# Optimization experiments

Measured on AMD Instinct MI355X. Metric: run time of the kernel, lower is better.

## Reference

```python
import jax, jax.numpy as jnp
import numpy as np

B = 1024        # graphs per batch
NPG = 64        # nodes per graph (uniform)
DEG = 16        # avg degree
NE_PG = 256     # candidate non-edges per graph
N = B * NPG
E = N * DEG
NE = B * NE_PG
EMB, HID, NCAT, NET, NOUT = 64, 128, 100, 4, 101  # NOUT = num_external + 1


def setup_inputs() -> dict:
    key = jax.random.key(0)
    ks = jax.random.split(key, 32)
    rn = lambda k, shape: jax.random.normal(k, shape, jnp.float32) * 0.05
    # graph structure: edges and non-edges stay within each graph's node block
    x = jax.random.randint(ks[0], (N,), 0, NCAT)
    offs = jnp.repeat(jnp.arange(B) * NPG, NPG * DEG)
    src = jax.random.randint(ks[1], (E,), 0, NPG) + offs
    dst = jax.random.randint(ks[2], (E,), 0, NPG) + offs
    edge_index = jnp.stack([src, dst])
    edge_attr = jax.random.randint(ks[3], (E,), 0, NET)
    offs_ne = jnp.repeat(jnp.arange(B) * NPG, NE_PG)
    non_edges = jax.random.randint(ks[4], (NE, 2), 0, NPG) + offs_ne[:, None]
    batch = jnp.repeat(jnp.arange(B), NPG)
    return dict(
        node_tab=rn(ks[5], (NCAT, EMB)), edge_tab=rn(ks[6], (NET, EMB)),
        c1_w=rn(ks[7], (EMB, HID)), c1_we=rn(ks[8], (EMB, HID)),
        c1_as=rn(ks[9], (HID,)), c1_ad=rn(ks[10], (HID,)), c1_ae=rn(ks[11], (HID,)), c1_b=rn(ks[12], (HID,)),
        c2_w=rn(ks[13], (HID, HID)), c2_we=rn(ks[14], (EMB, HID)),
        c2_as=rn(ks[15], (HID,)), c2_ad=rn(ks[16], (HID,)), c2_ae=rn(ks[17], (HID,)), c2_b=rn(ks[18], (HID,)),
        s_w1=rn(ks[19], (HID, HID)), s_b1=rn(ks[20], (HID,)), s_w2=rn(ks[21], (HID, 1)), s_b2=rn(ks[22], (1,)),
        n_w1=rn(ks[23], (HID, HID)), n_b1=rn(ks[24], (HID,)), n_w2=rn(ks[25], (HID, NOUT)), n_b2=rn(ks[26], (NOUT,)),
        e_w1=rn(ks[27], (HID, HID)), e_b1=rn(ks[28], (HID,)), e_w2=rn(ks[29], (HID, 1)), e_b2=rn(ks[30], (1,)),
        x=x, edge_index=edge_index, edge_attr=edge_attr, non_edges=non_edges, batch=batch,
    )


def _gat(h_in, src, dst, e, W, We, a_s, a_d, a_e, b):
    """PyG GATConv, heads=1: gather -> leakyrelu logits -> segment softmax over dst -> scatter sum."""
    n = h_in.shape[0]
    h = h_in @ W                  # [N, C]
    he = e @ We                   # [E, C]
    logit = (h @ a_s)[src] + (h @ a_d)[dst] + he @ a_e   # [E]
    logit = jnp.where(logit > 0, logit, 0.2 * logit)      # leaky_relu(0.2)
    m = jax.ops.segment_max(logit, dst, num_segments=n)
    ex = jnp.exp(logit - m[dst])
    den = jax.ops.segment_sum(ex, dst, num_segments=n)
    alpha = ex / (den[dst] + 1e-16)
    return jax.ops.segment_sum(h[src] * alpha[:, None], dst, num_segments=n) + b


def _mlp(z, w1, b1, w2, b2):
    return jax.nn.relu(z @ w1 + b1) @ w2 + b2


def reference(node_tab, edge_tab,
              c1_w, c1_we, c1_as, c1_ad, c1_ae, c1_b,
              c2_w, c2_we, c2_as, c2_ad, c2_ae, c2_b,
              s_w1, s_b1, s_w2, s_b2,
              n_w1, n_b1, n_w2, n_b2,
              e_w1, e_b1, e_w2, e_b2,
              x, edge_index, edge_attr, non_edges, batch):
    src, dst = edge_index[0], edge_index[1]
    e = edge_tab[edge_attr]                      # [E, EMB]
    h = node_tab[x]                              # [N, EMB]
    h = jax.nn.relu(_gat(h, src, dst, e, c1_w, c1_we, c1_as, c1_ad, c1_ae, c1_b))
    h = _gat(h, src, dst, e, c2_w, c2_we, c2_as, c2_ad, c2_ae, c2_b)   # [N, HID]
    g = jax.ops.segment_sum(h, batch, num_segments=B)                   # [B, HID]
    stop = _mlp(g, s_w1, s_b1, s_w2, s_b2)                              # [B, 1]
    addnode = _mlp(h, n_w1, n_b1, n_w2, n_b2)                           # [N, NOUT]
    pair = h[non_edges[:, 0]] + h[non_edges[:, 1]]                      # [NE, HID]
    addedge = _mlp(pair, e_w1, e_b1, e_w2, e_b2)                        # [NE, 1]
    # uniform per-graph sizes -> the torch split/pad is a static reshape+concat
    return jnp.concatenate(
        [stop, addnode.reshape(B, NPG * NOUT), addedge.reshape(B, NE_PG)], axis=1)
```

## Files before the change

### kernel.cpp

```cpp
#include <hip/hip_runtime.h>
#include <hip/hip_bf16.h>


#define NPG 64
#define EPG 1024
#define NEPG 256
#define B_GR 1024
#define E_TOT 1048576
#define EMB 64
#define HID 128
#define NOUT 101
#define OUT_PG 6721

typedef __attribute__((ext_vector_type(8))) short bf16x8;
typedef __attribute__((ext_vector_type(4))) float f32x4;
typedef unsigned short ushort_t;

__device__ ushort_t g_nt1[100*HID];
__device__ ushort_t g_c2w[HID*HID];
__device__ ushort_t g_nw1[HID*HID];
__device__ ushort_t g_ew1[HID*HID];
__device__ ushort_t g_nw2[HID*112];
__device__ float    g_sw1t[HID*HID];
__device__ float    g_hs1[128], g_hd1[128];
__device__ float    g_he1[4], g_he2[4];

__device__ __forceinline__ ushort_t f2bf(float f) {
  unsigned u = __float_as_uint(f);
  return (ushort_t)((u + 0x7fffu + ((u >> 16) & 1u)) >> 16);
}
__device__ __forceinline__ float bf2f(ushort_t h) {
  return __uint_as_float(((unsigned)h) << 16);
}
__device__ __forceinline__ unsigned pk2(float a, float b) {
  __hip_bfloat162 h = __float22bfloat162_rn(make_float2(a, b));
  unsigned r; __builtin_memcpy(&r, &h, 4); return r;
}
__device__ __forceinline__ bf16x8 pk8(float4 v0, float4 v1) {
  union { bf16x8 v; unsigned u[4]; } o;
  o.u[0] = pk2(v0.x, v0.y); o.u[1] = pk2(v0.z, v0.w);
  o.u[2] = pk2(v1.x, v1.y); o.u[3] = pk2(v1.z, v1.w);
  return o.v;
}

__global__ void prep_kernel(
    const float* __restrict__ node_tab, const float* __restrict__ edge_tab,
    const float* __restrict__ c1_w,  const float* __restrict__ c1_we,
    const float* __restrict__ c1_as, const float* __restrict__ c1_ad,
    const float* __restrict__ c1_ae,
    const float* __restrict__ c2_w,  const float* __restrict__ c2_we,
    const float* __restrict__ c2_ae,
    const float* __restrict__ s_w1,  const float* __restrict__ n_w1,
    const float* __restrict__ n_w2,  const float* __restrict__ e_w1)
{
  const int b = blockIdx.x, tid = threadIdx.x;
  if (b == 0) {
    __shared__ float v1[EMB], v2[EMB];
    if (tid < EMB) {
      float a = 0.f, d = 0.f;
      for (int j = 0; j < HID; ++j) {
        a = fmaf(c1_we[tid*HID + j], c1_ae[j], a);
        d = fmaf(c2_we[tid*HID + j], c2_ae[j], d);
      }
      v1[tid] = a; v2[tid] = d;
    }
    __syncthreads();
    if (tid < 4) {
      float a = 0.f, d = 0.f;
      for (int k = 0; k < EMB; ++k) {
        const float ev = edge_tab[tid*EMB + k];
        a = fmaf(ev, v1[k], a); d = fmaf(ev, v2[k], d);
      }
      g_he1[tid] = a; g_he2[tid] = d;
    }
    return;
  }
  if (b <= 50) {
    const int idx = (b - 1) * 256 + tid;
    const int i = idx >> 7, j = idx & (HID - 1);
    float s = 0.f;
    #pragma unroll 8
    for (int k = 0; k < EMB; ++k) s = fmaf(node_tab[i*EMB + k], c1_w[k*HID + j], s);
    g_nt1[idx] = f2bf(s);
    return;
  }
  if (b == 51) {
    __shared__ float vs[EMB], vd[EMB];
    if (tid < EMB) {
      float a = 0.f, d = 0.f;
      for (int j = 0; j < HID; ++j) {
        const float w = c1_w[tid*HID + j];
        a = fmaf(w, c1_as[j], a); d = fmaf(w, c1_ad[j], d);
      }
      vs[tid] = a; vd[tid] = d;
    }
    __syncthreads();
    if (tid < 128) {
      float a = 0.f, d = 0.f;
      if (tid < 100) {
        for (int k = 0; k < EMB; ++k) {
          const float xv = node_tab[tid*EMB + k];
          a = fmaf(xv, vs[k], a); d = fmaf(xv, vd[k], d);
        }
      }
      g_hs1[tid] = a; g_hd1[tid] = d;
    }
    return;
  }
  if (b <= 75) {
    const int grp = (b - 52) >> 3;
    const int chunk = (b - 52) & 7;
    const float* W = (grp == 0) ? c2_w : (grp == 1) ? n_w1 : e_w1;
    ushort_t* G = (grp == 0) ? g_c2w : (grp == 1) ? g_nw1 : g_ew1;
    const int base = chunk * 2048 + tid;
    #pragma unroll
    for (int it = 0; it < 8; ++it) {
      const int idx = base + it*256;
      const int j = idx & 7, l = (idx >> 3) & 63, r2 = idx >> 9;
      const int ks = r2 & 3, ct = r2 >> 2;
      const int row = ks*32 + (l >> 4)*8 + j;
      const int col = ct*16 + (l & 15);
      G[idx] = f2bf(W[row*HID + col]);
    }
    return;
  }
  if (b <= 82) {
    const int base = (b - 76) * 2048 + tid;
    #pragma unroll
    for (int it = 0; it < 8; ++it) {
      const int idx = base + it*256;
      const int j = idx & 7, l = (idx >> 3) & 63, r2 = idx >> 9;
      const int ks = r2 & 3, ct = r2 >> 2;
      const int row = ks*32 + (l >> 4)*8 + j;
      const int col = ct*16 + (l & 15);
      g_nw2[idx] = (col < NOUT) ? f2bf(n_w2[row*NOUT + col]) : (ushort_t)0;
    }
    return;
  }
  {
    const int base = (b - 83) * 2048 + tid;
    #pragma unroll
    for (int it = 0; it < 8; ++it) {
      const int idx = base + it*256;
      g_sw1t[idx] = s_w1[(idx & 127)*HID + (idx >> 7)];
    }
  }
}

#define S_HC   0
#define S_R    18432
#define S_PART 35840
#define S_NS   36864
#define S_ND   37120
#define S_GP   37376
#define S_EBW  37888
#define S_HCC  38912
#define S_XS   38944
#define S_TOT  39200

__global__ __launch_bounds__(256, 4) void graph_kernel(
    const float* __restrict__ c1_b,
    const float* __restrict__ c2_as, const float* __restrict__ c2_ad,
    const float* __restrict__ c2_b,
    const float* __restrict__ s_b1,  const float* __restrict__ s_w2,
    const float* __restrict__ s_b2,
    const float* __restrict__ n_b1,  const float* __restrict__ n_b2,
    const float* __restrict__ e_b1,  const float* __restrict__ e_w2,
    const float* __restrict__ e_b2,
    const int* __restrict__ x,  const int* __restrict__ ei,
    const int* __restrict__ ea, const int* __restrict__ nedg,
    float* __restrict__ out)
{
  const int tid = threadIdx.x;
  const int gid = blockIdx.x;
  const int nb = gid * NPG;
  const int lane = tid & 63;
  const int wv = tid >> 6;
  const int qd = lane >> 4;
  const int cl = lane & 15;
  const int rb = wv * 16;

  __shared__ __align__(16) char smem[S_TOT];
  ushort_t* Hc   = (ushort_t*)(smem + S_HC);
  float*    Pf   = (float*)   (smem + S_R);
  ushort_t* Hr   = (ushort_t*)(smem + S_R);
  float*    part = (float*)   (smem + S_PART);
  float*    ns   = (float*)   (smem + S_NS);
  float*    nd   = (float*)   (smem + S_ND);
  float*    gp   = (float*)   (smem + S_GP);
  float*    ebw  = (float*)   (smem + S_EBW);
  float*    hc   = (float*)   (smem + S_HCC);
  int*      xs   = (int*)     (smem + S_XS);
  ushort_t* a1b  = Hc;

  unsigned er[4];
  #pragma unroll
  for (int i = 0; i < 4; ++i) {
    const int k = tid + 256*i;
    const int s = ei[gid*EPG + k] - nb;
    const int d = ei[E_TOT + gid*EPG + k] - nb;
    const int t = ea[gid*EPG + k];
    er[i] = (unsigned)(s | (d << 6) | (t << 12));
  }
  const int2 prr = *(const int2*)(nedg + 2*(gid*NEPG + tid));
  if (tid < NPG) {
    const int cat = x[nb + tid];
    xs[tid] = cat;
    ns[tid] = g_hs1[cat];
    nd[tid] = g_hd1[cat];
  }
  {
    float4* pz = (float4*)Pf;
    #pragma unroll
    for (int j = 0; j < 4; ++j) pz[tid + j*256] = make_float4(0.f,0.f,0.f,0.f);
  }
  if (tid < 128) gp[tid] = 0.f;
  ebw[tid] = (tid < 128) ? e_b1[tid] : e_w2[tid - 128];
  if (tid < 8) hc[tid] = (tid < 4) ? g_he1[tid] : g_he2[tid-4];
  __syncthreads();

  {
    const int gn = tid >> 2;
    const int f0 = (tid & 3) * 32;
    const ushort_t* srcp = g_nt1 + xs[gn]*HID + f0;
    const bf16x8 t0 = ((const bf16x8*)srcp)[0];
    const bf16x8 t1 = ((const bf16x8*)srcp)[1];
    const bf16x8 t2 = ((const bf16x8*)srcp)[2];
    const bf16x8 t3 = ((const bf16x8*)srcp)[3];
    #pragma unroll
    for (int i = 0; i < 4; ++i) {
      const unsigned tp = er[i];
      const int s = tp & 63, d = (tp >> 6) & 63, t = tp >> 12;
      float l = ns[s] + nd[d] + hc[t];
      l = (l > 0.f) ? l : 0.2f * l;
      atomicAdd(&Pf[d*64 + s], __expf(l));
    }
    #pragma unroll
    for (int q = 0; q < 8; ++q) {
      Hc[(f0 +      q)*72 + gn] = (ushort_t)t0[q];
      Hc[(f0 +  8 + q)*72 + gn] = (ushort_t)t1[q];
      Hc[(f0 + 16 + q)*72 + gn] = (ushort_t)t2[q];
      Hc[(f0 + 24 + q)*72 + gn] = (ushort_t)t3[q];
    }
  }
  __syncthreads();

  bf16x8 pa0, pa1;
  float inv4[4];
  {
    const float* pr = Pf + (rb + cl)*64;
    const float4 v0 = *(const float4*)(pr + qd*8);
    const float4 v1 = *(const float4*)(pr + qd*8 + 4);
    const float4 v2 = *(const float4*)(pr + 32 + qd*8);
    const float4 v3 = *(const float4*)(pr + 36 + qd*8);
    pa0 = pk8(v0, v1); pa1 = pk8(v2, v3);
    float den = v0.x+v0.y+v0.z+v0.w + v1.x+v1.y+v1.z+v1.w
              + v2.x+v2.y+v2.z+v2.w + v3.x+v3.y+v3.z+v3.w;
    den += __shfl_xor(den, 16, 64);
    den += __shfl_xor(den, 32, 64);
    #pragma unroll
    for (int r = 0; r < 4; ++r)
      inv4[r] = 1.f / (__shfl(den, qd*4 + r, 64) + 1e-16f);
  }
  __syncthreads();

  {
    #pragma unroll
    for (int ct = 0; ct < 8; ++ct) {
      f32x4 acc = {0.f, 0.f, 0.f, 0.f};
      const bf16x8 b0 = *(const bf16x8*)(Hc + (ct*16+cl)*72 + qd*8);
      const bf16x8 b1 = *(const bf16x8*)(Hc + (ct*16+cl)*72 + 32 + qd*8);
      acc = __builtin_amdgcn_mfma_f32_16x16x32_bf16(pa0, b0, acc, 0, 0, 0);
      acc = __builtin_amdgcn_mfma_f32_16x16x32_bf16(pa1, b1, acc, 0, 0, 0);
      const int n = ct*16 + cl;
      const float bias = c1_b[n];
      #pragma unroll
      for (int r = 0; r < 4; ++r)
        Hr[(rb + qd*4 + r)*136 + n] = f2bf(fmaxf(fmaf(acc[r], inv4[r], bias), 0.f));
    }
  }
  bf16x8 h1f[4];
  #pragma unroll
  for (int ks = 0; ks < 4; ++ks)
    h1f[ks] = *(const bf16x8*)(Hr + (rb+cl)*136 + ks*32 + qd*8);
  __syncthreads();

  {
    float4* pz = (float4*)Pf;
    #pragma unroll
    for (int j = 0; j < 4; ++j) pz[tid + j*256] = make_float4(0.f,0.f,0.f,0.f);
    float pns[4] = {0.f,0.f,0.f,0.f}, pnd[4] = {0.f,0.f,0.f,0.f};
    #pragma unroll
    for (int ct = 0; ct < 8; ++ct) {
      f32x4 acc = {0.f, 0.f, 0.f, 0.f};
      #pragma unroll
      for (int ks = 0; ks < 4; ++ks) {
        const bf16x8 b = *(const bf16x8*)(g_c2w + ((ct*4+ks)*64 + lane)*8);
        acc = __builtin_amdgcn_mfma_f32_16x16x32_bf16(h1f[ks], b, acc, 0, 0, 0);
      }
      const int n = ct*16 + cl;
      const float asv = c2_as[n], adv = c2_ad[n];
      #pragma unroll
      for (int r = 0; r < 4; ++r) {
        const float v = acc[r];
        Hc[n*72 + (rb + qd*4 + r)] = f2bf(v);
        pns[r] = fmaf(v, asv, pns[r]);
        pnd[r] = fmaf(v, adv, pnd[r]);
      }
    }
    #pragma unroll
    for (int r = 0; r < 4; ++r) {
      #pragma unroll
      for (int off = 1; off < 16; off <<= 1) {
        pns[r] += __shfl_xor(pns[r], off, 64);
        pnd[r] += __shfl_xor(pnd[r], off, 64);
      }
    }
    if (cl == 0) {
      #pragma unroll
      for (int r = 0; r < 4; ++r) { ns[rb+qd*4+r] = pns[r]; nd[rb+qd*4+r] = pnd[r]; }
    }
  }
  __syncthreads();

  #pragma unroll
  for (int i = 0; i < 4; ++i) {
    const unsigned tp = er[i];
    const int s = tp & 63, d = (tp >> 6) & 63, t = tp >> 12;
    float l = ns[s] + nd[d] + hc[4 + t];
    l = (l > 0.f) ? l : 0.2f * l;
    atomicAdd(&Pf[d*64 + s], __expf(l));
  }
  __syncthreads();

  {
    const float* pr = Pf + (rb + cl)*64;
    const float4 v0 = *(const float4*)(pr + qd*8);
    const float4 v1 = *(const float4*)(pr + qd*8 + 4);
    const float4 v2 = *(const float4*)(pr + 32 + qd*8);
    const float4 v3 = *(const float4*)(pr + 36 + qd*8);
    pa0 = pk8(v0, v1); pa1 = pk8(v2, v3);
    float den = v0.x+v0.y+v0.z+v0.w + v1.x+v1.y+v1.z+v1.w
              + v2.x+v2.y+v2.z+v2.w + v3.x+v3.y+v3.z+v3.w;
    den += __shfl_xor(den, 16, 64);
    den += __shfl_xor(den, 32, 64);
    #pragma unroll
    for (int r = 0; r < 4; ++r)
      inv4[r] = 1.f / (__shfl(den, qd*4 + r, 64) + 1e-16f);
  }
  __syncthreads();

  {
    #pragma unroll
    for (int ct = 0; ct < 8; ++ct) {
      f32x4 acc = {0.f, 0.f, 0.f, 0.f};
      const bf16x8 b0 = *(const bf16x8*)(Hc + (ct*16+cl)*72 + qd*8);
      const bf16x8 b1 = *(const bf16x8*)(Hc + (ct*16+cl)*72 + 32 + qd*8);
      acc = __builtin_amdgcn_mfma_f32_16x16x32_bf16(pa0, b0, acc, 0, 0, 0);
      acc = __builtin_amdgcn_mfma_f32_16x16x32_bf16(pa1, b1, acc, 0, 0, 0);
      const int n = ct*16 + cl;
      const float bias = c2_b[n];
      float colsum = 0.f;
      #pragma unroll
      for (int r = 0; r < 4; ++r) {
        const float v = fmaf(acc[r], inv4[r], bias);
        Hr[(rb + qd*4 + r)*136 + n] = f2bf(v);
        colsum += v;
      }
      colsum += __shfl_xor(colsum, 16, 64);
      colsum += __shfl_xor(colsum, 32, 64);
      if (qd == 0) atomicAdd(&gp[n], colsum);
    }
  }
  __syncthreads();

  {
    const int j = tid & 127, half = tid >> 7;
    const float* wr = g_sw1t + j*HID + half*64;
    const float* gr = gp + half*64;
    float p = 0.f;
    #pragma unroll
    for (int q = 0; q < 16; ++q) {
      const float4 w = ((const float4*)wr)[q];
      const float4 g = ((const float4*)gr)[q];
      p = fmaf(w.x, g.x, p); p = fmaf(w.y, g.y, p);
      p = fmaf(w.z, g.z, p); p = fmaf(w.w, g.w, p);
    }
    part[tid] = p;
  }
  __syncthreads();

  if (tid < 64) {
    const float z0 = fmaxf(part[tid] + part[tid+128] + s_b1[tid], 0.f);
    const float z1 = fmaxf(part[tid+64] + part[tid+192] + s_b1[tid+64], 0.f);
    float p = fmaf(z0, s_w2[tid], z1 * s_w2[tid+64]);
    #pragma unroll
    for (int off = 32; off > 0; off >>= 1) p += __shfl_down(p, off, 64);
    if (tid == 0) out[(size_t)gid*OUT_PG] = p + s_b2[0];
  }

  bf16x8 h2f[4];
  #pragma unroll
  for (int ks = 0; ks < 4; ++ks)
    h2f[ks] = *(const bf16x8*)(Hr + (rb+cl)*136 + ks*32 + qd*8);

  {
    #pragma unroll
    for (int ct = 0; ct < 8; ++ct) {
      f32x4 an = {0.f, 0.f, 0.f, 0.f};
      f32x4 ae2 = {0.f, 0.f, 0.f, 0.f};
      #pragma unroll
      for (int ks = 0; ks < 4; ++ks) {
        const bf16x8 bn = *(const bf16x8*)(g_nw1 + ((ct*4+ks)*64 + lane)*8);
        const bf16x8 be = *(const bf16x8*)(g_ew1 + ((ct*4+ks)*64 + lane)*8);
        an  = __builtin_amdgcn_mfma_f32_16x16x32_bf16(h2f[ks], bn, an, 0, 0, 0);
        ae2 = __builtin_amdgcn_mfma_f32_16x16x32_bf16(h2f[ks], be, ae2, 0, 0, 0);
      }
      const int n = ct*16 + cl;
      const float bias = n_b1[n];
      #pragma unroll
      for (int r = 0; r < 4; ++r) {
        a1b[(rb + qd*4 + r)*136 + n] = f2bf(fmaxf(an[r] + bias, 0.f));
        Hr[(rb + qd*4 + r)*136 + n] = f2bf(ae2[r]);
      }
    }
  }
  {
    bf16x8 af[4];
    #pragma unroll
    for (int ks = 0; ks < 4; ++ks)
      af[ks] = *(const bf16x8*)(a1b + (rb+cl)*136 + ks*32 + qd*8);
    float* ob = out + (size_t)gid*OUT_PG + 1;
    #pragma unroll
    for (int ct = 0; ct < 7; ++ct) {
      f32x4 acc = {0.f, 0.f, 0.f, 0.f};
      #pragma unroll
      for (int ks = 0; ks < 4; ++ks) {
        const bf16x8 b = *(const bf16x8*)(g_nw2 + ((ct*4+ks)*64 + lane)*8);
        acc = __builtin_amdgcn_mfma_f32_16x16x32_bf16(af[ks], b, acc, 0, 0, 0);
      }
      const int o = ct*16 + cl;
      if (o < NOUT) {
        const float b2 = n_b2[o];
        #pragma unroll
        for (int r = 0; r < 4; ++r)
          ob[(size_t)(rb + qd*4 + r)*NOUT + o] = acc[r] + b2;
      }
    }
  }
  __syncthreads();

  {
    const ushort_t* ui = Hr + (prr.x - nb)*136;
    const ushort_t* uj = Hr + (prr.y - nb)*136;
    float ssum = 0.f;
    #pragma unroll
    for (int q8 = 0; q8 < 16; ++q8) {
      const bf16x8 va = *(const bf16x8*)(ui + q8*8);
      const bf16x8 vb = *(const bf16x8*)(uj + q8*8);
      #pragma unroll
      for (int j = 0; j < 8; ++j) {
        const int c = q8*8 + j;
        float v = bf2f((ushort_t)va[j]) + bf2f((ushort_t)vb[j]) + ebw[c];
        v = fmaxf(v, 0.f);
        ssum = fmaf(v, ebw[128 + c], ssum);
      }
    }
    out[(size_t)gid*OUT_PG + 1 + NPG*NOUT + tid] = ssum + e_b2[0];
  }
}

extern "C" void kernel_launch(void* const* d_in, const int* in_sizes, int n_in,
                              void* d_out, int out_size, void* d_ws, size_t ws_size,
                              hipStream_t stream) {
  const float* node_tab = (const float*)d_in[0];
  const float* edge_tab = (const float*)d_in[1];
  const float* c1_w  = (const float*)d_in[2];
  const float* c1_we = (const float*)d_in[3];
  const float* c1_as = (const float*)d_in[4];
  const float* c1_ad = (const float*)d_in[5];
  const float* c1_ae = (const float*)d_in[6];
  const float* c1_b  = (const float*)d_in[7];
  const float* c2_w  = (const float*)d_in[8];
  const float* c2_we = (const float*)d_in[9];
  const float* c2_as = (const float*)d_in[10];
  const float* c2_ad = (const float*)d_in[11];
  const float* c2_ae = (const float*)d_in[12];
  const float* c2_b  = (const float*)d_in[13];
  const float* s_w1  = (const float*)d_in[14];
  const float* s_b1  = (const float*)d_in[15];
  const float* s_w2  = (const float*)d_in[16];
  const float* s_b2  = (const float*)d_in[17];
  const float* n_w1  = (const float*)d_in[18];
  const float* n_b1  = (const float*)d_in[19];
  const float* n_w2  = (const float*)d_in[20];
  const float* n_b2  = (const float*)d_in[21];
  const float* e_w1  = (const float*)d_in[22];
  const float* e_b1  = (const float*)d_in[23];
  const float* e_w2  = (const float*)d_in[24];
  const float* e_b2  = (const float*)d_in[25];
  const int* x    = (const int*)d_in[26];
  const int* ei   = (const int*)d_in[27];
  const int* ea   = (const int*)d_in[28];
  const int* nedg = (const int*)d_in[29];
  float* out = (float*)d_out;

  prep_kernel<<<dim3(91), dim3(256), 0, stream>>>(
      node_tab, edge_tab, c1_w, c1_we, c1_as, c1_ad, c1_ae,
      c2_w, c2_we, c2_ae, s_w1, n_w1, n_w2, e_w1);

  graph_kernel<<<dim3(B_GR), dim3(256), 0, stream>>>(
      c1_b, c2_as, c2_ad, c2_b, s_b1, s_w2, s_b2,
      n_b1, n_b2, e_b1, e_w2, e_b2, x, ei, ea, nedg, out);
}
```

Before: 185.5 us.

## Double block to 512 threads splitting column tiles across wave pairs, swizzle score matrix

Doubles the per-graph thread block from 256 to 512 threads. Each pair of wave groups now handles half the output column tiles in every MFMA stage, and the per-edge, non-edge and stop-MLP work is split over twice as many threads, with partial sums combined through atomics, shuffles or extra reductions. It also XOR-swizzles the attention score matrix layout in shared memory to cut bank conflicts on the atomic adds and row reads. The aim is more parallelism per graph to hide latency, at the cost of extra barriers, some shared-memory atomics, and launch bounds asking for 8 blocks per CU, which tightens register limits.

```diff
diff --git a/kernel.cpp b/kernel.cpp
--- a/kernel.cpp
+++ b/kernel.cpp
@@ -41,6 +41,9 @@
   o.u[0] = pk2(v0.x, v0.y); o.u[1] = pk2(v0.z, v0.w);
   o.u[2] = pk2(v1.x, v1.y); o.u[3] = pk2(v1.z, v1.w);
   return o.v;
+}
+__device__ __forceinline__ int pf_idx(int d, int s) {
+  return d*64 + ((((s >> 2) ^ d) & 15) << 2) + (s & 3);
 }
 
 __global__ void prep_kernel(
@@ -150,15 +153,15 @@
 #define S_HC   0
 #define S_R    18432
 #define S_PART 35840
-#define S_NS   36864
-#define S_ND   37120
-#define S_GP   37376
-#define S_EBW  37888
-#define S_HCC  38912
-#define S_XS   38944
-#define S_TOT  39200
-
-__global__ __launch_bounds__(256, 4) void graph_kernel(
+#define S_NS   37888
+#define S_ND   38144
+#define S_GP   38400
+#define S_EBW  38912
+#define S_HCC  39936
+#define S_XS   39968
+#define S_TOT  40224
+
+__global__ __launch_bounds__(512, 8) void graph_kernel(
     const float* __restrict__ c1_b,
     const float* __restrict__ c2_as, const float* __restrict__ c2_ad,
     const float* __restrict__ c2_b,
@@ -176,9 +179,11 @@
   const int nb = gid * NPG;
   const int lane = tid & 63;
   const int wv = tid >> 6;
+  const int wr = wv & 3;
+  const int ch = wv >> 2;
   const int qd = lane >> 4;
   const int cl = lane & 15;
-  const int rb = wv * 16;
+  const int rb = wr * 16;
 
   __shared__ __align__(16) char smem[S_TOT];
   ushort_t* Hc   = (ushort_t*)(smem + S_HC);
@@ -193,16 +198,16 @@
   int*      xs   = (int*)     (smem + S_XS);
   ushort_t* a1b  = Hc;
 
-  unsigned er[4];
+  unsigned er[2];
   #pragma unroll
-  for (int i = 0; i < 4; ++i) {
-    const int k = tid + 256*i;
+  for (int i = 0; i < 2; ++i) {
+    const int k = tid + 512*i;
     const int s = ei[gid*EPG + k] - nb;
     const int d = ei[E_TOT + gid*EPG + k] - nb;
     const int t = ea[gid*EPG + k];
     er[i] = (unsigned)(s | (d << 6) | (t << 12));
   }
-  const int2 prr = *(const int2*)(nedg + 2*(gid*NEPG + tid));
+  const int2 prr = *(const int2*)(nedg + 2*(gid*NEPG + (tid >> 1)));
   if (tid < NPG) {
     const int cat = x[nb + tid];
     xs[tid] = cat;
@@ -211,36 +216,31 @@
   }
   {
     float4* pz = (float4*)Pf;
-    #pragma unroll
-    for (int j = 0; j < 4; ++j) pz[tid + j*256] = make_float4(0.f,0.f,0.f,0.f);
+    pz[tid]       = make_float4(0.f,0.f,0.f,0.f);
+    pz[tid + 512] = make_float4(0.f,0.f,0.f,0.f);
   }
   if (tid < 128) gp[tid] = 0.f;
-  ebw[tid] = (tid < 128) ? e_b1[tid] : e_w2[tid - 128];
+  if (tid < 256) ebw[tid] = (tid < 128) ? e_b1[tid] : e_w2[tid - 128];
   if (tid < 8) hc[tid] = (tid < 4) ? g_he1[tid] : g_he2[tid-4];
   __syncthreads();
 
   {
-    const int gn = tid >> 2;
-    const int f0 = (tid & 3) * 32;
-    const ushort_t* srcp = g_nt1 + xs[gn]*HID + f0;
+    const int f0 = wv * 16;
+    const ushort_t* srcp = g_nt1 + xs[lane]*HID + f0;
     const bf16x8 t0 = ((const bf16x8*)srcp)[0];
     const bf16x8 t1 = ((const bf16x8*)srcp)[1];
-    const bf16x8 t2 = ((const bf16x8*)srcp)[2];
-    const bf16x8 t3 = ((const bf16x8*)srcp)[3];
-    #pragma unroll
-    for (int i = 0; i < 4; ++i) {
+    #pragma unroll
+    for (int i = 0; i < 2; ++i) {
       const unsigned tp = er[i];
       const int s = tp & 63, d = (tp >> 6) & 63, t = tp >> 12;
       float l = ns[s] + nd[d] + hc[t];
       l = (l > 0.f) ? l : 0.2f * l;
-      atomicAdd(&Pf[d*64 + s], __expf(l));
+      atomicAdd(&Pf[pf_idx(d, s)], __expf(l));
     }
     #pragma unroll
     for (int q = 0; q < 8; ++q) {
-      Hc[(f0 +      q)*72 + gn] = (ushort_t)t0[q];
-      Hc[(f0 +  8 + q)*72 + gn] = (ushort_t)t1[q];
-      Hc[(f0 + 16 + q)*72 + gn] = (ushort_t)t2[q];
-      Hc[(f0 + 24 + q)*72 + gn] = (ushort_t)t3[q];
+      Hc[(f0 +     q)*72 + lane] = (ushort_t)t0[q];
+      Hc[(f0 + 8 + q)*72 + lane] = (ushort_t)t1[q];
     }
   }
   __syncthreads();
@@ -249,10 +249,10 @@
   float inv4[4];
   {
     const float* pr = Pf + (rb + cl)*64;
-    const float4 v0 = *(const float4*)(pr + qd*8);
-    const float4 v1 = *(const float4*)(pr + qd*8 + 4);
-    const float4 v2 = *(const float4*)(pr + 32 + qd*8);
-    const float4 v3 = *(const float4*)(pr + 36 + qd*8);
+    const float4 v0 = *(const float4*)(pr + (((2*qd    ) ^ cl) << 2));
+    const float4 v1 = *(const float4*)(pr + (((2*qd + 1) ^ cl) << 2));
+    const float4 v2 = *(const float4*)(pr + (((2*qd + 8) ^ cl) << 2));
+    const float4 v3 = *(const float4*)(pr + (((2*qd + 9) ^ cl) << 2));
     pa0 = pk8(v0, v1); pa1 = pk8(v2, v3);
     float den = v0.x+v0.y+v0.z+v0.w + v1.x+v1.y+v1.z+v1.w
               + v2.x+v2.y+v2.z+v2.w + v3.x+v3.y+v3.z+v3.w;
@@ -262,11 +262,13 @@
     for (int r = 0; r < 4; ++r)
       inv4[r] = 1.f / (__shfl(den, qd*4 + r, 64) + 1e-16f);
   }
-  __syncthreads();
-
-  {
-    #pragma unroll
-    for (int ct = 0; ct < 8; ++ct) {
+  if (tid < NPG) { ns[tid] = 0.f; nd[tid] = 0.f; }
+  __syncthreads();
+
+  {
+    #pragma unroll
+    for (int i = 0; i < 4; ++i) {
+      const int ct = ch*4 + i;
       f32x4 acc = {0.f, 0.f, 0.f, 0.f};
       const bf16x8 b0 = *(const bf16x8*)(Hc + (ct*16+cl)*72 + qd*8);
       const bf16x8 b1 = *(const bf16x8*)(Hc + (ct*16+cl)*72 + 32 + qd*8);
@@ -279,6 +281,7 @@
         Hr[(rb + qd*4 + r)*136 + n] = f2bf(fmaxf(fmaf(acc[r], inv4[r], bias), 0.f));
     }
   }
+  __syncthreads();
   bf16x8 h1f[4];
   #pragma unroll
   for (int ks = 0; ks < 4; ++ks)
@@ -287,11 +290,12 @@
 
   {
     float4* pz = (float4*)Pf;
-    #pragma unroll
-    for (int j = 0; j < 4; ++j) pz[tid + j*256] = make_float4(0.f,0.f,0.f,0.f);
+    pz[tid]       = make_float4(0.f,0.f,0.f,0.f);
+    pz[tid + 512] = make_float4(0.f,0.f,0.f,0.f);
     float pns[4] = {0.f,0.f,0.f,0.f}, pnd[4] = {0.f,0.f,0.f,0.f};
     #pragma unroll
-    for (int ct = 0; ct < 8; ++ct) {
+    for (int i = 0; i < 4; ++i) {
+      const int ct = ch*4 + i;
       f32x4 acc = {0.f, 0.f, 0.f, 0.f};
       #pragma unroll
       for (int ks = 0; ks < 4; ++ks) {
@@ -318,27 +322,30 @@
     }
     if (cl == 0) {
       #pragma unroll
-      for (int r = 0; r < 4; ++r) { ns[rb+qd*4+r] = pns[r]; nd[rb+qd*4+r] = pnd[r]; }
+      for (int r = 0; r < 4; ++r) {
+        atomicAdd(&ns[rb + qd*4 + r], pns[r]);
+        atomicAdd(&nd[rb + qd*4 + r], pnd[r]);
+      }
     }
   }
   __syncthreads();
 
   #pragma unroll
-  for (int i = 0; i < 4; ++i) {
+  for (int i = 0; i < 2; ++i) {
     const unsigned tp = er[i];
     const int s = tp & 63, d = (tp >> 6) & 63, t = tp >> 12;
     float l = ns[s] + nd[d] + hc[4 + t];
     l = (l > 0.f) ? l : 0.2f * l;
-    atomicAdd(&Pf[d*64 + s], __expf(l));
+    atomicAdd(&Pf[pf_idx(d, s)], __expf(l));
   }
   __syncthreads();
 
   {
     const float* pr = Pf + (rb + cl)*64;
-    const float4 v0 = *(const float4*)(pr + qd*8);
-    const float4 v1 = *(const float4*)(pr + qd*8 + 4);
-    const float4 v2 = *(const float4*)(pr + 32 + qd*8);
-    const float4 v3 = *(const float4*)(pr + 36 + qd*8);
+    const float4 v0 = *(const float4*)(pr + (((2*qd    ) ^ cl) << 2));
+    const float4 v1 = *(const float4*)(pr + (((2*qd + 1) ^ cl) << 2));
+    const float4 v2 = *(const float4*)(pr + (((2*qd + 8) ^ cl) << 2));
+    const float4 v3 = *(const float4*)(pr + (((2*qd + 9) ^ cl) << 2));
     pa0 = pk8(v0, v1); pa1 = pk8(v2, v3);
     float den = v0.x+v0.y+v0.z+v0.w + v1.x+v1.y+v1.z+v1.w
               + v2.x+v2.y+v2.z+v2.w + v3.x+v3.y+v3.z+v3.w;
@@ -352,7 +359,8 @@
 
   {
     #pragma unroll
-    for (int ct = 0; ct < 8; ++ct) {
+    for (int i = 0; i < 4; ++i) {
+      const int ct = ch*4 + i;
       f32x4 acc = {0.f, 0.f, 0.f, 0.f};
       const bf16x8 b0 = *(const bf16x8*)(Hc + (ct*16+cl)*72 + qd*8);
       const bf16x8 b1 = *(const bf16x8*)(Hc + (ct*16+cl)*72 + 32 + qd*8);
@@ -375,39 +383,41 @@
   __syncthreads();
 
   {
-    const int j = tid & 127, half = tid >> 7;
-    const float* wr = g_sw1t + j*HID + half*64;
-    const float* gr = gp + half*64;
+    const int j = tid & 127, c = tid >> 7;
+    const float* wrp = g_sw1t + j*HID + c*32;
+    const float* grp = gp + c*32;
     float p = 0.f;
     #pragma unroll
-    for (int q = 0; q < 16; ++q) {
-      const float4 w = ((const float4*)wr)[q];
-      const float4 g = ((const float4*)gr)[q];
+    for (int q = 0; q < 8; ++q) {
+      const float4 w = ((const float4*)wrp)[q];
+      const float4 g = ((const float4*)grp)[q];
       p = fmaf(w.x, g.x, p); p = fmaf(w.y, g.y, p);
       p = fmaf(w.z, g.z, p); p = fmaf(w.w, g.w, p);
     }
     part[tid] = p;
   }
-  __syncthreads();
-
-  if (tid < 64) {
-    const float z0 = fmaxf(part[tid] + part[tid+128] + s_b1[tid], 0.f);
-    const float z1 = fmaxf(part[tid+64] + part[tid+192] + s_b1[tid+64], 0.f);
-    float p = fmaf(z0, s_w2[tid], z1 * s_w2[tid+64]);
-    #pragma unroll
-    for (int off = 32; off > 0; off >>= 1) p += __shfl_down(p, off, 64);
-    if (tid == 0) out[(size_t)gid*OUT_PG] = p + s_b2[0];
-  }
-
   bf16x8 h2f[4];
   #pragma unroll
   for (int ks = 0; ks < 4; ++ks)
     h2f[ks] = *(const bf16x8*)(Hr + (rb+cl)*136 + ks*32 + qd*8);
-
-  {
-    #pragma unroll
-    for (int ct = 0; ct < 8; ++ct) {
-      f32x4 an = {0.f, 0.f, 0.f, 0.f};
+  __syncthreads();
+
+  if (tid < 64) {
+    const float d0 = part[tid]    + part[tid+128] + part[tid+256] + part[tid+384];
+    const float d1 = part[tid+64] + part[tid+192] + part[tid+320] + part[tid+448];
+    const float z0 = fmaxf(d0 + s_b1[tid], 0.f);
+    const float z1 = fmaxf(d1 + s_b1[tid+64], 0.f);
+    float p = fmaf(z0, s_w2[tid], z1 * s_w2[tid+64]);
+    #pragma unroll
+    for (int off = 32; off > 0; off >>= 1) p += __shfl_down(p, off, 64);
+    if (tid == 0) out[(size_t)gid*OUT_PG] = p + s_b2[0];
+  }
+
+  {
+    #pragma unroll
+    for (int i = 0; i < 4; ++i) {
+      const int ct = ch*4 + i;
+      f32x4 an  = {0.f, 0.f, 0.f, 0.f};
       f32x4 ae2 = {0.f, 0.f, 0.f, 0.f};
       #pragma unroll
       for (int ks = 0; ks < 4; ++ks) {
@@ -425,6 +435,8 @@
       }
     }
   }
+  __syncthreads();
+
   {
     bf16x8 af[4];
     #pragma unroll
@@ -432,41 +444,47 @@
       af[ks] = *(const bf16x8*)(a1b + (rb+cl)*136 + ks*32 + qd*8);
     float* ob = out + (size_t)gid*OUT_PG + 1;
     #pragma unroll
-    for (int ct = 0; ct < 7; ++ct) {
-      f32x4 acc = {0.f, 0.f, 0.f, 0.f};
-      #pragma unroll
-      for (int ks = 0; ks < 4; ++ks) {
-        const bf16x8 b = *(const bf16x8*)(g_nw2 + ((ct*4+ks)*64 + lane)*8);
-        acc = __builtin_amdgcn_mfma_f32_16x16x32_bf16(af[ks], b, acc, 0, 0, 0);
-      }
-      const int o = ct*16 + cl;
-      if (o < NOUT) {
-        const float b2 = n_b2[o];
+    for (int i = 0; i < 4; ++i) {
+      const int ct = ch*4 + i;
+      if (ct < 7) {
+        f32x4 acc = {0.f, 0.f, 0.f, 0.f};
         #pragma unroll
-        for (int r = 0; r < 4; ++r)
-          ob[(size_t)(rb + qd*4 + r)*NOUT + o] = acc[r] + b2;
-      }
-    }
-  }
-  __syncthreads();
-
-  {
-    const ushort_t* ui = Hr + (prr.x - nb)*136;
-    const ushort_t* uj = Hr + (prr.y - nb)*136;
+        for (int ks = 0; ks < 4; ++ks) {
+          const bf16x8 b = *(const bf16x8*)(g_nw2 + ((ct*4+ks)*64 + lane)*8);
+          acc = __builtin_amdgcn_mfma_f32_16x16x32_bf16(af[ks], b, acc, 0, 0, 0);
+        }
+        const int o = ct*16 + cl;
+        if (o < NOUT) {
+          const float b2 = n_b2[o];
+          #pragma unroll
+          for (int r = 0; r < 4; ++r)
+            ob[(size_t)(rb + qd*4 + r)*NOUT + o] = acc[r] + b2;
+        }
+      }
+    }
+  }
+  __syncthreads();
+
+  {
+    const int pi = tid >> 1, hf = tid & 1;
+    const ushort_t* ui = Hr + (prr.x - nb)*136 + hf*64;
+    const ushort_t* uj = Hr + (prr.y - nb)*136 + hf*64;
     float ssum = 0.f;
     #pragma unroll
-    for (int q8 = 0; q8 < 16; ++q8) {
+    for (int q8 = 0; q8 < 8; ++q8) {
       const bf16x8 va = *(const bf16x8*)(ui + q8*8);
       const bf16x8 vb = *(const bf16x8*)(uj + q8*8);
       #pragma unroll
       for (int j = 0; j < 8; ++j) {
-        const int c = q8*8 + j;
+        const int c = hf*64 + q8*8 + j;
         float v = bf2f((ushort_t)va[j]) + bf2f((ushort_t)vb[j]) + ebw[c];
         v = fmaxf(v, 0.f);
         ssum = fmaf(v, ebw[128 + c], ssum);
       }
     }
-    out[(size_t)gid*OUT_PG + 1 + NPG*NOUT + tid] = ssum + e_b2[0];
+    ssum += __shfl_xor(ssum, 1, 64);
+    if (hf == 0)
+      out[(size_t)gid*OUT_PG + 1 + NPG*NOUT + pi] = ssum + e_b2[0];
   }
 }
 
@@ -509,7 +527,7 @@
       node_tab, edge_tab, c1_w, c1_we, c1_as, c1_ad, c1_ae,
       c2_w, c2_we, c2_ae, s_w1, n_w1, n_w2, e_w1);
 
-  graph_kernel<<<dim3(B_GR), dim3(256), 0, stream>>>(
+  graph_kernel<<<dim3(B_GR), dim3(512), 0, stream>>>(
       c1_b, c2_as, c2_ad, c2_b, s_b1, s_w2, s_b2,
       n_b1, n_b2, e_b1, e_w2, e_b2, x, ei, ea, nedg, out);
 }
```

After: 185.2 us. No clear change (-0.2%).
